# Optimization experiments

Hardware: AMD Instinct MI355X
Metric: run time of the kernel (lower is better)

The kernel has to match this reference:

```python
import jax, jax.numpy as jnp
import numpy as np

N_GENES = 978

def setup_inputs() -> dict:
    key = jax.random.key(0)
    ks = jax.random.split(key, 8)
    B = 8192
    N = B * N_GENES  # 8,009,856 nodes
    E = 20_000_000
    inputs = jax.random.normal(ks[0], (B, N_GENES), dtype=jnp.float32)
    edges = jax.random.randint(ks[1], (2, E), 0, N, dtype=jnp.int64)
    gcn_w = jax.random.normal(ks[2], (1, 1), dtype=jnp.float32)
    gcn_b = jax.random.normal(ks[3], (1,), dtype=jnp.float32)
    W1 = jax.random.normal(ks[4], (N_GENES, 2048), dtype=jnp.float32) * 0.03
    b1 = jax.random.normal(ks[5], (2048,), dtype=jnp.float32) * 0.01
    W2 = jax.random.normal(ks[6], (2048, 100), dtype=jnp.float32) * 0.02
    b2 = jax.random.normal(ks[7], (100,), dtype=jnp.float32) * 0.01
    return {"inputs": inputs, "edges": edges, "gcn_w": gcn_w, "gcn_b": gcn_b,
            "W1": W1, "b1": b1, "W2": W2, "b2": b2}

def reference(inputs, edges, gcn_w, gcn_b, W1, b1, W2, b2):
    B = inputs.shape[0]
    N = B * N_GENES
    # GCNConv(1,1, add_self_loops=False, normalize=False):
    # x' = x * w; out[dst] = sum over edges of x'[src]; out += bias
    x = inputs.reshape(-1) * gcn_w[0, 0]            # [N] node scalars
    src, dst = edges[0], edges[1]                   # messages flow src -> dst
    agg = jax.ops.segment_sum(x[src], dst, num_segments=N)  # irregular scatter-add
    agg = agg + gcn_b[0]
    h = agg.reshape(B, N_GENES)
    h = jax.nn.relu(h)                              # dropout = identity (eval)
    h = jax.nn.relu(h @ W1 + b1)                    # [B, 2048]
    out = h @ W2 + b2                               # [B, 100]
    return out
```

## Files before the change

kernel.cpp:

```cpp
#include <hip/hip_runtime.h>
#include <hip/hip_bf16.h>
#include <stdint.h>


typedef unsigned short u16;
typedef unsigned int u32;
typedef __bf16 bf16x8 __attribute__((ext_vector_type(8)));
typedef float f32x4 __attribute__((ext_vector_type(4)));

#define NGENES 978
#define KPAD   1024
#define H1DIM  2048
#define NOUT   100
#define NOUTP  112
#define KSPLIT 8

#define NB      978
#define BSH     13
#define BNODES  8192
#define NWG_BIN 2048
#define SC_WGS  256
#define SC_THR  512
#define SDEPTH  32
#define OVFCAP  256

__device__ __forceinline__ u16 f2b(float f) {
    unsigned u = __builtin_bit_cast(unsigned, f);
    u = (u + 0x7FFFu + ((u >> 16) & 1u)) >> 16;
    return (u16)u;
}

__device__ __forceinline__ u32 nt_u32(const u32* p) {
    return __builtin_nontemporal_load(p);
}
__device__ __forceinline__ float nt_f32(const float* p) {
    return __builtin_nontemporal_load(p);
}

__device__ __forceinline__ void gl2lds16(const void* g, void* l) {
    __builtin_amdgcn_global_load_lds(
        (const __attribute__((address_space(1))) void*)(uintptr_t)g,
        (__attribute__((address_space(3))) void*)(unsigned)(uintptr_t)l,
        16, 0, 0);
}

__global__ void detect_kernel(const unsigned* __restrict__ e, int* __restrict__ flag) {
    if (threadIdx.x == 0) {
        int is64 = 1;
        for (int i = 0; i < 64; ++i) {
            if (e[2 * i + 1] != 0u) { is64 = 0; break; }
        }
        *flag = is64;
    }
}

__global__ void xbf_kernel(const float* __restrict__ x, const float* __restrict__ gcn_w,
                           u16* __restrict__ xb, int N) {
    const float w = gcn_w[0];
    int i = (blockIdx.x * 256 + threadIdx.x) * 4;
    if (i + 3 < N) {
        float4 v = *(const float4*)&x[i];
        xb[i + 0] = f2b(v.x * w);
        xb[i + 1] = f2b(v.y * w);
        xb[i + 2] = f2b(v.z * w);
        xb[i + 3] = f2b(v.w * w);
    } else {
        for (int k = i; k < N; ++k) xb[k] = f2b(x[k] * w);
    }
}

__global__ __launch_bounds__(256) void hist_kernel(const void* __restrict__ edges,
                                                   const int* __restrict__ flag, int E,
                                                   u32* __restrict__ hist) {
    __shared__ u32 h[NB];
    for (int i = threadIdx.x; i < NB; i += 256) h[i] = 0;
    __syncthreads();
    const int wg = blockIdx.x;
    const int per = (E + NWG_BIN - 1) / NWG_BIN;
    const int s = wg * per;
    const int e = min(E, s + per);
    const u32* eb = (const u32*)edges;
    const int st = (*flag) ? 2 : 1;
    const u32* dp = eb + (size_t)st * E;
    int i = s + threadIdx.x;
    for (; i + 7 * 256 < e; i += 8 * 256) {
        u32 d[8];
#pragma unroll
        for (int k = 0; k < 8; ++k) d[k] = nt_u32(&dp[(size_t)st * (i + k * 256)]);
#pragma unroll
        for (int k = 0; k < 8; ++k) atomicAdd(&h[d[k] >> BSH], 1u);
    }
    for (; i < e; i += 256) atomicAdd(&h[nt_u32(&dp[(size_t)st * i]) >> BSH], 1u);
    __syncthreads();
    for (int b = threadIdx.x; b < NB; b += 256) hist[(size_t)b * NWG_BIN + wg] = h[b];
}

__global__ void scan_wg_kernel(u32* __restrict__ hist, u32* __restrict__ totals) {
    const int b = blockIdx.x;
    u32* row = hist + (size_t)b * NWG_BIN;
    const int lane = threadIdx.x;
    u32 running = 0;
#pragma unroll
    for (int it = 0; it < NWG_BIN / 64; ++it) {
        u32 raw = row[it * 64 + lane];
        u32 v = (raw + 15u) & ~15u;
        u32 incl = v;
#pragma unroll
        for (int off = 1; off < 64; off <<= 1) {
            u32 t = __shfl_up(incl, off, 64);
            if (lane >= off) incl += t;
        }
        row[it * 64 + lane] = running + incl - v;
        running += __shfl(incl, 63, 64);
    }
    if (lane == 0) totals[b] = running;
}

__global__ void scan_bucket_kernel(const u32* __restrict__ totals, u32* __restrict__ bases) {
    const int lane = threadIdx.x;
    u32 running = 0;
    const int iters = (NB + 63) / 64;
    for (int it = 0; it < iters; ++it) {
        int idx = it * 64 + lane;
        u32 v = (idx < NB) ? totals[idx] : 0;
        u32 incl = v;
#pragma unroll
        for (int off = 1; off < 64; off <<= 1) {
            u32 t = __shfl_up(incl, off, 64);
            if (lane >= off) incl += t;
        }
        if (idx < NB) bases[idx] = running + incl - v;
        running += __shfl(incl, 63, 64);
    }
    if (lane == 0) bases[NB] = running;
}

__global__ __launch_bounds__(SC_THR) void binscatter_kernel(const void* __restrict__ edges,
                                                            const u16* __restrict__ xb,
                                                            const int* __restrict__ flag, int E,
                                                            const u32* __restrict__ hist,
                                                            const u32* __restrict__ bases,
                                                            u32* __restrict__ pairs) {
    __shared__ u32 cur[NB];
    __shared__ u32 sfill[NB];
    __shared__ u32 stage[NB * SDEPTH];
    __shared__ u32 ovf[OVFCAP * 2];
    __shared__ u32 ocount;
    const int tid = threadIdx.x;
    const int wg = blockIdx.x;
    for (int b = tid; b < NB; b += SC_THR) {
        cur[b] = bases[b] + hist[(size_t)b * NWG_BIN + wg * (NWG_BIN / SC_WGS)];
        sfill[b] = 0;
    }
    if (tid == 0) ocount = 0;
    __syncthreads();

    const int per = (E + NWG_BIN - 1) / NWG_BIN;
    const int s = wg * (NWG_BIN / SC_WGS) * per;
    const int e = min(E, s + (NWG_BIN / SC_WGS) * per);
    const u32* eb = (const u32*)edges;
    const int st = (*flag) ? 2 : 1;
    const u32* sp = eb;
    const u32* dp = eb + (size_t)st * E;

    for (int base_i = s; base_i < e; base_i += 8 * SC_THR) {
        const int idx = base_i + tid;
        u32 srcv[8], dv[8];
        u16 val[8];
#pragma unroll
        for (int k = 0; k < 8; ++k) {
            int i = idx + k * SC_THR;
            bool ok = i < e;
            srcv[k] = ok ? nt_u32(&sp[(size_t)st * i]) : 0u;
            dv[k]   = ok ? nt_u32(&dp[(size_t)st * i]) : 0xFFFFFFFFu;
        }
#pragma unroll
        for (int k = 0; k < 8; ++k)
            val[k] = (dv[k] != 0xFFFFFFFFu) ? xb[srcv[k]] : (u16)0;

#pragma unroll
        for (int h = 0; h < 2; ++h) {
#pragma unroll
            for (int k = 4 * h; k < 4 * h + 4; ++k) {
                if (dv[k] != 0xFFFFFFFFu) {
                    u32 b = dv[k] >> BSH;
                    u32 pr = ((dv[k] & (BNODES - 1)) << 16) | (u32)val[k];
                    u32 slot = atomicAdd(&sfill[b], 1u);
                    if (slot < SDEPTH) {
                        stage[b * SDEPTH + slot] = pr;
                    } else {
                        atomicSub(&sfill[b], 1u);
                        u32 o = atomicAdd(&ocount, 1u);
                        if (o < OVFCAP) { ovf[o * 2] = b; ovf[o * 2 + 1] = pr; }
                    }
                }
            }
            __syncthreads();
            for (int b = tid; b < NB; b += SC_THR) {
                u32 f = sfill[b];
                u32 nl = f >> 4;
                if (nl) {
                    u32 wbase = cur[b];
                    u32 n16 = nl << 4;
                    for (u32 j = 0; j < n16; j += 4)
                        *(uint4*)&pairs[wbase + j] = *(const uint4*)&stage[b * SDEPTH + j];
                    u32 rem = f & 15u;
                    for (u32 r = 0; r < rem; ++r)
                        stage[b * SDEPTH + r] = stage[b * SDEPTH + n16 + r];
                    cur[b] = wbase + n16;
                    sfill[b] = rem;
                }
            }
            __syncthreads();
            u32 oc = ocount;
            if (oc) {
                if (tid < oc && tid < OVFCAP) {
                    u32 b = ovf[tid * 2];
                    u32 pr = ovf[tid * 2 + 1];
                    u32 slot = atomicAdd(&sfill[b], 1u);
                    stage[b * SDEPTH + slot] = pr;
                }
                __syncthreads();
                if (tid == 0) ocount = 0;
                __syncthreads();
            }
        }
    }
    for (int b = tid; b < NB; b += SC_THR) {
        u32 f = sfill[b];
        if (f) {
            u32 wbase = cur[b];
            u32 padded = (f + 15u) & ~15u;
            for (u32 j = 0; j < padded; j += 4) {
                uint4 v;
                v.x = (j + 0 < f) ? stage[b * SDEPTH + j + 0] : 0u;
                v.y = (j + 1 < f) ? stage[b * SDEPTH + j + 1] : 0u;
                v.z = (j + 2 < f) ? stage[b * SDEPTH + j + 2] : 0u;
                v.w = (j + 3 < f) ? stage[b * SDEPTH + j + 3] : 0u;
                *(uint4*)&pairs[wbase + j] = v;
            }
        }
    }
}

__global__ __launch_bounds__(512) void accum_kernel(const u32* __restrict__ pairs,
                                                    const u32* __restrict__ bases,
                                                    float* __restrict__ agg) {
    __shared__ float acc[BNODES];
    for (int i = threadIdx.x; i < BNODES; i += 512) acc[i] = 0.f;
    __syncthreads();
    const int b = blockIdx.x;
    const u32 p0 = bases[b], p1 = bases[b + 1];
    u32 p = p0 + threadIdx.x;
    for (; p + 3 * 512 < p1; p += 4 * 512) {
        u32 pk[4];
#pragma unroll
        for (int k = 0; k < 4; ++k) pk[k] = nt_u32(&pairs[p + k * 512]);
#pragma unroll
        for (int k = 0; k < 4; ++k) {
            float v = __builtin_bit_cast(float, (pk[k] & 0xFFFFu) << 16);
            atomicAdd(&acc[pk[k] >> 16], v);
        }
    }
    for (; p < p1; p += 512) {
        u32 pk = nt_u32(&pairs[p]);
        float v = __builtin_bit_cast(float, (pk & 0xFFFFu) << 16);
        atomicAdd(&acc[pk >> 16], v);
    }
    __syncthreads();
    const size_t node0 = (size_t)b << BSH;
    for (int i = threadIdx.x; i < BNODES; i += 512) agg[node0 + i] = acc[i];
}

__global__ void scatter_kernel(const void* __restrict__ edges, const float* __restrict__ x,
                               const float* __restrict__ gcn_w, float* __restrict__ agg,
                               const int* __restrict__ flag, int E) {
    long long e = (long long)blockIdx.x * 256 + threadIdx.x;
    if (e >= E) return;
    int s, d;
    if (*flag) {
        const long long* e64 = (const long long*)edges;
        s = (int)e64[e];
        d = (int)e64[(long long)E + e];
    } else {
        const int* e32 = (const int*)edges;
        s = e32[e];
        d = e32[(long long)E + e];
    }
    atomicAdd(&agg[d], x[s] * gcn_w[0]);
}

__global__ void act_kernel(const float* __restrict__ agg, const float* __restrict__ gcn_b,
                           u16* __restrict__ A) {
    int idx = blockIdx.x * 256 + threadIdx.x;
    int i = idx >> 10;
    int k = idx & 1023;
    float v = 0.f;
    if (k < NGENES) {
        v = nt_f32(&agg[(size_t)i * NGENES + k]) + gcn_b[0];
        v = v > 0.f ? v : 0.f;
    }
    A[idx] = f2b(v);
}

__global__ void transposeW1(const float* __restrict__ W1, u16* __restrict__ W1T) {
    __shared__ float t[32][33];
    int n0 = blockIdx.x * 32;
    int k0 = blockIdx.y * 32;
    int tx = threadIdx.x, ty = threadIdx.y;
    for (int r = ty; r < 32; r += 8) {
        int k = k0 + r;
        t[r][tx] = (k < NGENES) ? W1[(size_t)k * H1DIM + n0 + tx] : 0.f;
    }
    __syncthreads();
    for (int r = ty; r < 32; r += 8) {
        int n = n0 + r;
        W1T[(size_t)n * KPAD + k0 + tx] = f2b(t[tx][r]);
    }
}

__global__ void transposeW2(const float* __restrict__ W2, u16* __restrict__ W2T) {
    __shared__ float t[32][33];
    int n0 = blockIdx.x * 32;
    int k0 = blockIdx.y * 32;
    int tx = threadIdx.x, ty = threadIdx.y;
    for (int r = ty; r < 32; r += 8) {
        int k = k0 + r;
        int n = n0 + tx;
        t[r][tx] = (n < NOUT) ? W2[(size_t)k * NOUT + n] : 0.f;
    }
    __syncthreads();
    for (int r = ty; r < 32; r += 8) {
        int n = n0 + r;
        if (n < NOUTP) W2T[(size_t)n * H1DIM + k0 + tx] = f2b(t[tx][r]);
    }
}

__global__ __launch_bounds__(256) void gemm1_kernel(const u16* __restrict__ A,
                                                    const u16* __restrict__ Bt,
                                                    const float* __restrict__ b1,
                                                    u16* __restrict__ H) {
    __shared__ u16 As[128 * 32];
    __shared__ u16 Bs[128 * 32];
    const int tid = threadIdx.x;
    const int m0 = blockIdx.y * 128;
    const int n0 = blockIdx.x * 128;
    const int wave = tid >> 6;
    const int lane = tid & 63;
    const int wm = (wave >> 1) * 64;
    const int wn = (wave & 1) * 64;
    const int quad = lane >> 4;
    const int l16 = lane & 15;

    f32x4 acc[4][4];
#pragma unroll
    for (int i = 0; i < 4; ++i)
#pragma unroll
        for (int j = 0; j < 4; ++j)
            acc[i][j] = (f32x4){0.f, 0.f, 0.f, 0.f};

    const int ch0 = tid, ch1 = tid + 256;
    const u16* ag0 = A + (size_t)(m0 + (ch0 >> 2)) * KPAD + (ch0 & 3) * 8;
    const u16* ag1 = A + (size_t)(m0 + (ch1 >> 2)) * KPAD + (ch1 & 3) * 8;
    const u16* bg0 = Bt + (size_t)(n0 + (ch0 >> 2)) * KPAD + (ch0 & 3) * 8;
    const u16* bg1 = Bt + (size_t)(n0 + (ch1 >> 2)) * KPAD + (ch1 & 3) * 8;
    u16* la0 = &As[ch0 * 8];
    u16* la1 = &As[ch1 * 8];
    u16* lb0 = &Bs[ch0 * 8];
    u16* lb1 = &Bs[ch1 * 8];

    for (int k0 = 0; k0 < KPAD; k0 += 32) {
        gl2lds16(ag0, la0);
        gl2lds16(ag1, la1);
        gl2lds16(bg0, lb0);
        gl2lds16(bg1, lb1);
        ag0 += 32; ag1 += 32; bg0 += 32; bg1 += 32;
        __syncthreads();

        bf16x8 af[4], bfr[4];
#pragma unroll
        for (int i = 0; i < 4; ++i)
            af[i] = *(const bf16x8*)&As[(wm + i * 16 + l16) * 32 + quad * 8];
#pragma unroll
        for (int j = 0; j < 4; ++j)
            bfr[j] = *(const bf16x8*)&Bs[(wn + j * 16 + l16) * 32 + quad * 8];
#pragma unroll
        for (int i = 0; i < 4; ++i)
#pragma unroll
            for (int j = 0; j < 4; ++j)
                acc[i][j] = __builtin_amdgcn_mfma_f32_16x16x32_bf16(af[i], bfr[j], acc[i][j], 0, 0, 0);
        __syncthreads();
    }

#pragma unroll
    for (int j = 0; j < 4; ++j) {
        const int col = n0 + wn + j * 16 + l16;
        const float bv = b1[col];
#pragma unroll
        for (int i = 0; i < 4; ++i) {
            const int rbase = m0 + wm + i * 16 + quad * 4;
#pragma unroll
            for (int r = 0; r < 4; ++r) {
                float v = acc[i][j][r] + bv;
                v = v > 0.f ? v : 0.f;
                H[(size_t)(rbase + r) * H1DIM + col] = f2b(v);
            }
        }
    }
}

__global__ __launch_bounds__(256) void gemm2_kernel(const u16* __restrict__ Hh,
                                                    const u16* __restrict__ W2T,
                                                    const float* __restrict__ b2,
                                                    float* __restrict__ out) {
    __shared__ u16 As[64 * 32];
    __shared__ u16 Bs[NOUTP * 32];
    const int tid = threadIdx.x;
    const int m0 = blockIdx.y * 64;
    const int kc = blockIdx.x;
    const int kbase = kc * (H1DIM / KSPLIT);
    const int wave = tid >> 6;
    const int lane = tid & 63;
    const int quad = lane >> 4;
    const int l16 = lane & 15;

    f32x4 acc[7];
#pragma unroll
    for (int j = 0; j < 7; ++j) acc[j] = (f32x4){0.f, 0.f, 0.f, 0.f};

    const u16* ag = Hh + (size_t)(m0 + (tid >> 2)) * H1DIM + kbase + (tid & 3) * 8;
    u16* la = &As[tid * 8];
    const u16* bg0 = W2T + (size_t)(tid >> 2) * H1DIM + kbase + (tid & 3) * 8;
    u16* lb0 = &Bs[tid * 8];
    const int ch1 = tid + 256;
    const u16* bg1 = W2T + (size_t)(ch1 >> 2) * H1DIM + kbase + (ch1 & 3) * 8;
    u16* lb1 = &Bs[ch1 * 8];
    const bool bact = (ch1 < NOUTP * 4);

    for (int kk = 0; kk < H1DIM / KSPLIT; kk += 32) {
        gl2lds16(ag, la);
        gl2lds16(bg0, lb0);
        if (bact) gl2lds16(bg1, lb1);
        ag += 32; bg0 += 32; bg1 += 32;
        __syncthreads();

        bf16x8 af = *(const bf16x8*)&As[(wave * 16 + l16) * 32 + quad * 8];
#pragma unroll
        for (int j = 0; j < 7; ++j) {
            bf16x8 bfr = *(const bf16x8*)&Bs[(j * 16 + l16) * 32 + quad * 8];
            acc[j] = __builtin_amdgcn_mfma_f32_16x16x32_bf16(af, bfr, acc[j], 0, 0, 0);
        }
        __syncthreads();
    }

#pragma unroll
    for (int j = 0; j < 7; ++j) {
        const int col = j * 16 + l16;
        if (col < NOUT) {
            const float bv = (kc == 0) ? b2[col] : 0.f;
            const int rbase = m0 + wave * 16 + quad * 4;
#pragma unroll
            for (int r = 0; r < 4; ++r)
                atomicAdd(&out[(size_t)(rbase + r) * NOUT + col], acc[j][r] + bv);
        }
    }
}

extern "C" void kernel_launch(void* const* d_in, const int* in_sizes, int n_in,
                              void* d_out, int out_size, void* d_ws, size_t ws_size,
                              hipStream_t stream) {
    const float* inputs = (const float*)d_in[0];
    const void*  edges  = d_in[1];
    const float* gcn_w  = (const float*)d_in[2];
    const float* gcn_b  = (const float*)d_in[3];
    const float* W1     = (const float*)d_in[4];
    const float* b1     = (const float*)d_in[5];
    const float* W2     = (const float*)d_in[6];
    const float* b2     = (const float*)d_in[7];
    float* out = (float*)d_out;

    const int N = in_sizes[0];
    const int Brows = N / NGENES;
    const int E = in_sizes[1] / 2;

    char* ws = (char*)d_ws;
    size_t off = 0;
    auto carve = [&](size_t bytes) -> void* {
        void* p = ws + off;
        off = (off + bytes + 255) & ~(size_t)255;
        return p;
    };
    float* agg = (float*)carve((size_t)N * 4);
    u16*   Abf = (u16*)carve((size_t)Brows * KPAD * 2);
    u16*   W1T = (u16*)carve((size_t)H1DIM * KPAD * 2);
    u16*   W2Tp = (u16*)carve((size_t)NOUTP * H1DIM * 2);
    u16*   H1  = (u16*)carve((size_t)Brows * H1DIM * 2);
    int*   flag = (int*)carve(256);
    u16*   xb     = (u16*)carve((size_t)N * 2);
    u32*   hist   = (u32*)carve((size_t)NB * NWG_BIN * 4);
    u32*   totals = (u32*)carve((size_t)NB * 4);
    u32*   bases  = (u32*)carve((size_t)(NB + 1) * 4);
    u32*   pairs  = (u32*)carve((size_t)E * 4 + ((size_t)16 << 20));
    const bool use_binned = (off <= ws_size);

    hipMemsetAsync(out, 0, (size_t)out_size * 4, stream);
    detect_kernel<<<1, 64, 0, stream>>>((const unsigned*)edges, flag);

    if (use_binned) {
        xbf_kernel<<<(N / 4 + 255) / 256, 256, 0, stream>>>(inputs, gcn_w, xb, N);
        hist_kernel<<<NWG_BIN, 256, 0, stream>>>(edges, flag, E, hist);
        scan_wg_kernel<<<NB, 64, 0, stream>>>(hist, totals);
        scan_bucket_kernel<<<1, 64, 0, stream>>>(totals, bases);
        binscatter_kernel<<<SC_WGS, SC_THR, 0, stream>>>(edges, xb, flag, E,
                                                         hist, bases, pairs);
        accum_kernel<<<NB, 512, 0, stream>>>(pairs, bases, agg);
    } else {
        hipMemsetAsync(agg, 0, (size_t)N * 4, stream);
        const int sblocks = (E + 255) / 256;
        scatter_kernel<<<sblocks, 256, 0, stream>>>(edges, inputs, gcn_w, agg, flag, E);
    }

    act_kernel<<<(Brows * KPAD) / 256, 256, 0, stream>>>(agg, gcn_b, Abf);

    transposeW1<<<dim3(H1DIM / 32, KPAD / 32), dim3(32, 8), 0, stream>>>(W1, W1T);
    transposeW2<<<dim3(4, H1DIM / 32), dim3(32, 8), 0, stream>>>(W2, W2Tp);

    gemm1_kernel<<<dim3(H1DIM / 128, Brows / 128), 256, 0, stream>>>(Abf, W1T, b1, H1);
    gemm2_kernel<<<dim3(KSPLIT, Brows / 64), 256, 0, stream>>>(H1, W2Tp, b2, out);
}
```

Before: 883.6 us.

## Replace histogram prefix-scan binning with fixed-capacity buckets and global atomic cursors

Removes the histogram pass and the two scan kernels. The scatter kernel now claims space in fixed-capacity per-bucket regions using global atomic counters, with a global overflow list fixed up by a small extra kernel. This saves one full read of the dst edge array plus the scan launches. The LDS stage is transposed to a slot-major layout, the scatter block grows to 1024 threads, and accumulation skips zero padding entries. In exchange it adds global atomics per 16-entry chunk, a larger pairs buffer, and correctness now depends on the capacity bounds, with buckets over capacity falling back to the overflow path.

After: 786.3 us. 1.12x faster.

```diff
diff --git a/kernel.cpp b/kernel.cpp
--- a/kernel.cpp
+++ b/kernel.cpp
@@ -18,11 +18,11 @@
 #define NB      978
 #define BSH     13
 #define BNODES  8192
-#define NWG_BIN 2048
 #define SC_WGS  256
-#define SC_THR  512
+#define SC_THR  1024
 #define SDEPTH  32
 #define OVFCAP  256
+#define CAP_B   24576
 
 __device__ __forceinline__ u16 f2b(float f) {
     unsigned u = __builtin_bit_cast(unsigned, f);
@@ -69,95 +69,25 @@
     }
 }
 
-__global__ __launch_bounds__(256) void hist_kernel(const void* __restrict__ edges,
-                                                   const int* __restrict__ flag, int E,
-                                                   u32* __restrict__ hist) {
-    __shared__ u32 h[NB];
-    for (int i = threadIdx.x; i < NB; i += 256) h[i] = 0;
-    __syncthreads();
-    const int wg = blockIdx.x;
-    const int per = (E + NWG_BIN - 1) / NWG_BIN;
-    const int s = wg * per;
-    const int e = min(E, s + per);
-    const u32* eb = (const u32*)edges;
-    const int st = (*flag) ? 2 : 1;
-    const u32* dp = eb + (size_t)st * E;
-    int i = s + threadIdx.x;
-    for (; i + 7 * 256 < e; i += 8 * 256) {
-        u32 d[8];
-#pragma unroll
-        for (int k = 0; k < 8; ++k) d[k] = nt_u32(&dp[(size_t)st * (i + k * 256)]);
-#pragma unroll
-        for (int k = 0; k < 8; ++k) atomicAdd(&h[d[k] >> BSH], 1u);
-    }
-    for (; i < e; i += 256) atomicAdd(&h[nt_u32(&dp[(size_t)st * i]) >> BSH], 1u);
-    __syncthreads();
-    for (int b = threadIdx.x; b < NB; b += 256) hist[(size_t)b * NWG_BIN + wg] = h[b];
-}
-
-__global__ void scan_wg_kernel(u32* __restrict__ hist, u32* __restrict__ totals) {
-    const int b = blockIdx.x;
-    u32* row = hist + (size_t)b * NWG_BIN;
-    const int lane = threadIdx.x;
-    u32 running = 0;
-#pragma unroll
-    for (int it = 0; it < NWG_BIN / 64; ++it) {
-        u32 raw = row[it * 64 + lane];
-        u32 v = (raw + 15u) & ~15u;
-        u32 incl = v;
-#pragma unroll
-        for (int off = 1; off < 64; off <<= 1) {
-            u32 t = __shfl_up(incl, off, 64);
-            if (lane >= off) incl += t;
-        }
-        row[it * 64 + lane] = running + incl - v;
-        running += __shfl(incl, 63, 64);
-    }
-    if (lane == 0) totals[b] = running;
-}
-
-__global__ void scan_bucket_kernel(const u32* __restrict__ totals, u32* __restrict__ bases) {
-    const int lane = threadIdx.x;
-    u32 running = 0;
-    const int iters = (NB + 63) / 64;
-    for (int it = 0; it < iters; ++it) {
-        int idx = it * 64 + lane;
-        u32 v = (idx < NB) ? totals[idx] : 0;
-        u32 incl = v;
-#pragma unroll
-        for (int off = 1; off < 64; off <<= 1) {
-            u32 t = __shfl_up(incl, off, 64);
-            if (lane >= off) incl += t;
-        }
-        if (idx < NB) bases[idx] = running + incl - v;
-        running += __shfl(incl, 63, 64);
-    }
-    if (lane == 0) bases[NB] = running;
-}
-
 __global__ __launch_bounds__(SC_THR) void binscatter_kernel(const void* __restrict__ edges,
                                                             const u16* __restrict__ xb,
                                                             const int* __restrict__ flag, int E,
-                                                            const u32* __restrict__ hist,
-                                                            const u32* __restrict__ bases,
-                                                            u32* __restrict__ pairs) {
-    __shared__ u32 cur[NB];
+                                                            u32* __restrict__ pairs,
+                                                            u32* __restrict__ cnt,
+                                                            u32* __restrict__ ovfg,
+                                                            u32* __restrict__ ovfcnt) {
     __shared__ u32 sfill[NB];
-    __shared__ u32 stage[NB * SDEPTH];
+    __shared__ u32 stage[SDEPTH * NB];
     __shared__ u32 ovf[OVFCAP * 2];
     __shared__ u32 ocount;
     const int tid = threadIdx.x;
-    const int wg = blockIdx.x;
-    for (int b = tid; b < NB; b += SC_THR) {
-        cur[b] = bases[b] + hist[(size_t)b * NWG_BIN + wg * (NWG_BIN / SC_WGS)];
-        sfill[b] = 0;
-    }
+    for (int b = tid; b < NB; b += SC_THR) sfill[b] = 0;
     if (tid == 0) ocount = 0;
     __syncthreads();
 
-    const int per = (E + NWG_BIN - 1) / NWG_BIN;
-    const int s = wg * (NWG_BIN / SC_WGS) * per;
-    const int e = min(E, s + (NWG_BIN / SC_WGS) * per);
+    const int per = (E + SC_WGS - 1) / SC_WGS;
+    const int s = blockIdx.x * per;
+    const int e = min(E, s + per);
     const u32* eb = (const u32*)edges;
     const int st = (*flag) ? 2 : 1;
     const u32* sp = eb;
@@ -187,11 +117,17 @@
                     u32 pr = ((dv[k] & (BNODES - 1)) << 16) | (u32)val[k];
                     u32 slot = atomicAdd(&sfill[b], 1u);
                     if (slot < SDEPTH) {
-                        stage[b * SDEPTH + slot] = pr;
+                        stage[slot * NB + b] = pr;
                     } else {
                         atomicSub(&sfill[b], 1u);
                         u32 o = atomicAdd(&ocount, 1u);
-                        if (o < OVFCAP) { ovf[o * 2] = b; ovf[o * 2 + 1] = pr; }
+                        if (o < OVFCAP) {
+                            ovf[o * 2] = b; ovf[o * 2 + 1] = pr;
+                        } else {
+                            u32 og = atomicAdd(ovfcnt, 1u);
+                            ovfg[og * 2] = (b << BSH) | (pr >> 16);
+                            ovfg[og * 2 + 1] = pr & 0xFFFFu;
+                        }
                     }
                 }
             }
@@ -200,25 +136,52 @@
                 u32 f = sfill[b];
                 u32 nl = f >> 4;
                 if (nl) {
-                    u32 wbase = cur[b];
+                    u32 base = atomicAdd(&cnt[b], nl << 4);
+                    for (u32 g = 0; g < nl; ++g) {
+                        u32 wb = base + (g << 4);
+                        if (wb < CAP_B) {
+                            u32* dst = &pairs[(size_t)b * CAP_B + wb];
+#pragma unroll
+                            for (int q = 0; q < 4; ++q) {
+                                uint4 v;
+                                v.x = stage[(g * 16 + q * 4 + 0) * NB + b];
+                                v.y = stage[(g * 16 + q * 4 + 1) * NB + b];
+                                v.z = stage[(g * 16 + q * 4 + 2) * NB + b];
+                                v.w = stage[(g * 16 + q * 4 + 3) * NB + b];
+                                *(uint4*)&dst[q * 4] = v;
+                            }
+                        } else {
+                            for (int q = 0; q < 16; ++q) {
+                                u32 pr = stage[(g * 16 + q) * NB + b];
+                                u32 og = atomicAdd(ovfcnt, 1u);
+                                ovfg[og * 2] = (b << BSH) | (pr >> 16);
+                                ovfg[og * 2 + 1] = pr & 0xFFFFu;
+                            }
+                        }
+                    }
                     u32 n16 = nl << 4;
-                    for (u32 j = 0; j < n16; j += 4)
-                        *(uint4*)&pairs[wbase + j] = *(const uint4*)&stage[b * SDEPTH + j];
                     u32 rem = f & 15u;
                     for (u32 r = 0; r < rem; ++r)
-                        stage[b * SDEPTH + r] = stage[b * SDEPTH + n16 + r];
-                    cur[b] = wbase + n16;
+                        stage[r * NB + b] = stage[(n16 + r) * NB + b];
                     sfill[b] = rem;
                 }
             }
             __syncthreads();
             u32 oc = ocount;
             if (oc) {
-                if (tid < oc && tid < OVFCAP) {
+                u32 m = oc < (u32)OVFCAP ? oc : (u32)OVFCAP;
+                if (tid < (int)m) {
                     u32 b = ovf[tid * 2];
                     u32 pr = ovf[tid * 2 + 1];
                     u32 slot = atomicAdd(&sfill[b], 1u);
-                    stage[b * SDEPTH + slot] = pr;
+                    if (slot < SDEPTH) {
+                        stage[slot * NB + b] = pr;
+                    } else {
+                        atomicSub(&sfill[b], 1u);
+                        u32 og = atomicAdd(ovfcnt, 1u);
+                        ovfg[og * 2] = (b << BSH) | (pr >> 16);
+                        ovfg[og * 2 + 1] = pr & 0xFFFFu;
+                    }
                 }
                 __syncthreads();
                 if (tid == 0) ocount = 0;
@@ -229,28 +192,46 @@
     for (int b = tid; b < NB; b += SC_THR) {
         u32 f = sfill[b];
         if (f) {
-            u32 wbase = cur[b];
             u32 padded = (f + 15u) & ~15u;
-            for (u32 j = 0; j < padded; j += 4) {
-                uint4 v;
-                v.x = (j + 0 < f) ? stage[b * SDEPTH + j + 0] : 0u;
-                v.y = (j + 1 < f) ? stage[b * SDEPTH + j + 1] : 0u;
-                v.z = (j + 2 < f) ? stage[b * SDEPTH + j + 2] : 0u;
-                v.w = (j + 3 < f) ? stage[b * SDEPTH + j + 3] : 0u;
-                *(uint4*)&pairs[wbase + j] = v;
+            u32 base = atomicAdd(&cnt[b], padded);
+            for (u32 g = 0; g < (padded >> 4); ++g) {
+                u32 wb = base + (g << 4);
+                if (wb < CAP_B) {
+                    u32* dst = &pairs[(size_t)b * CAP_B + wb];
+#pragma unroll
+                    for (int q = 0; q < 4; ++q) {
+                        uint4 v;
+                        u32 j = g * 16 + q * 4;
+                        v.x = (j + 0 < f) ? stage[(j + 0) * NB + b] : 0u;
+                        v.y = (j + 1 < f) ? stage[(j + 1) * NB + b] : 0u;
+                        v.z = (j + 2 < f) ? stage[(j + 2) * NB + b] : 0u;
+                        v.w = (j + 3 < f) ? stage[(j + 3) * NB + b] : 0u;
+                        *(uint4*)&dst[q * 4] = v;
+                    }
+                } else {
+                    for (u32 q = g * 16; q < f && q < g * 16 + 16; ++q) {
+                        u32 pr = stage[q * NB + b];
+                        u32 og = atomicAdd(ovfcnt, 1u);
+                        ovfg[og * 2] = (b << BSH) | (pr >> 16);
+                        ovfg[og * 2 + 1] = pr & 0xFFFFu;
+                    }
+                }
             }
         }
     }
 }
 
 __global__ __launch_bounds__(512) void accum_kernel(const u32* __restrict__ pairs,
-                                                    const u32* __restrict__ bases,
+                                                    const u32* __restrict__ cnt,
                                                     float* __restrict__ agg) {
     __shared__ float acc[BNODES];
     for (int i = threadIdx.x; i < BNODES; i += 512) acc[i] = 0.f;
     __syncthreads();
     const int b = blockIdx.x;
-    const u32 p0 = bases[b], p1 = bases[b + 1];
+    u32 n = cnt[b];
+    if (n > CAP_B) n = CAP_B;
+    const u32 p0 = (u32)b * CAP_B;
+    const u32 p1 = p0 + n;
     u32 p = p0 + threadIdx.x;
     for (; p + 3 * 512 < p1; p += 4 * 512) {
         u32 pk[4];
@@ -258,18 +239,31 @@
         for (int k = 0; k < 4; ++k) pk[k] = nt_u32(&pairs[p + k * 512]);
 #pragma unroll
         for (int k = 0; k < 4; ++k) {
-            float v = __builtin_bit_cast(float, (pk[k] & 0xFFFFu) << 16);
-            atomicAdd(&acc[pk[k] >> 16], v);
+            if (pk[k]) {
+                float v = __builtin_bit_cast(float, (pk[k] & 0xFFFFu) << 16);
+                atomicAdd(&acc[pk[k] >> 16], v);
+            }
         }
     }
     for (; p < p1; p += 512) {
         u32 pk = nt_u32(&pairs[p]);
-        float v = __builtin_bit_cast(float, (pk & 0xFFFFu) << 16);
-        atomicAdd(&acc[pk >> 16], v);
+        if (pk) {
+            float v = __builtin_bit_cast(float, (pk & 0xFFFFu) << 16);
+            atomicAdd(&acc[pk >> 16], v);
+        }
     }
     __syncthreads();
     const size_t node0 = (size_t)b << BSH;
     for (int i = threadIdx.x; i < BNODES; i += 512) agg[node0 + i] = acc[i];
+}
+
+__global__ void ovf_fix_kernel(const u32* __restrict__ ovfg, const u32* __restrict__ ovfcnt,
+                               float* __restrict__ agg) {
+    u32 n = *ovfcnt;
+    for (u32 i = blockIdx.x * 256 + threadIdx.x; i < n; i += gridDim.x * 256) {
+        float v = __builtin_bit_cast(float, ovfg[i * 2 + 1] << 16);
+        atomicAdd(&agg[ovfg[i * 2]], v);
+    }
 }
 
 __global__ void scatter_kernel(const void* __restrict__ edges, const float* __restrict__ x,
@@ -497,23 +491,22 @@
     u16*   H1  = (u16*)carve((size_t)Brows * H1DIM * 2);
     int*   flag = (int*)carve(256);
     u16*   xb     = (u16*)carve((size_t)N * 2);
-    u32*   hist   = (u32*)carve((size_t)NB * NWG_BIN * 4);
-    u32*   totals = (u32*)carve((size_t)NB * 4);
-    u32*   bases  = (u32*)carve((size_t)(NB + 1) * 4);
-    u32*   pairs  = (u32*)carve((size_t)E * 4 + ((size_t)16 << 20));
+    u32*   cnt    = (u32*)carve((size_t)(NB + 64) * 4);
+    u32*   ovfcnt = cnt + NB;
+    u32*   ovfg   = (u32*)carve((size_t)(1 << 20) * 8);
+    u32*   pairs  = (u32*)carve((size_t)NB * CAP_B * 4);
     const bool use_binned = (off <= ws_size);
 
     hipMemsetAsync(out, 0, (size_t)out_size * 4, stream);
     detect_kernel<<<1, 64, 0, stream>>>((const unsigned*)edges, flag);
 
     if (use_binned) {
+        hipMemsetAsync(cnt, 0, (size_t)(NB + 64) * 4, stream);
         xbf_kernel<<<(N / 4 + 255) / 256, 256, 0, stream>>>(inputs, gcn_w, xb, N);
-        hist_kernel<<<NWG_BIN, 256, 0, stream>>>(edges, flag, E, hist);
-        scan_wg_kernel<<<NB, 64, 0, stream>>>(hist, totals);
-        scan_bucket_kernel<<<1, 64, 0, stream>>>(totals, bases);
         binscatter_kernel<<<SC_WGS, SC_THR, 0, stream>>>(edges, xb, flag, E,
-                                                         hist, bases, pairs);
-        accum_kernel<<<NB, 512, 0, stream>>>(pairs, bases, agg);
+                                                         pairs, cnt, ovfg, ovfcnt);
+        accum_kernel<<<NB, 512, 0, stream>>>(pairs, cnt, agg);
+        ovf_fix_kernel<<<8, 256, 0, stream>>>(ovfg, ovfcnt, agg);
     } else {
         hipMemsetAsync(agg, 0, (size_t)N * 4, stream);
         const int sblocks = (E + 255) / 256;
```
